# Kernel tuning notes

Measured on AMD Instinct MI355X. Metric: run time of the kernel, lower is better.

## Reference

```python
import jax, jax.numpy as jnp
import numpy as np

B, S, D, H = 4, 2048, 1024, 16
HD = D // H          # head_dim = 64; per-head scale = sqrt(HD) as in source
FF = 4096
EPS = 1e-5


def _layernorm(x, g, b):
    m = jnp.mean(x, axis=-1, keepdims=True)
    v = jnp.mean(jnp.square(x - m), axis=-1, keepdims=True)
    return (x - m) * jax.lax.rsqrt(v + EPS) * g + b


def setup_inputs() -> dict:
    key = jax.random.key(0)
    ks = jax.random.split(key, 10)
    std = 0.02
    return {
        "x": jax.random.normal(ks[0], (B, S, D), jnp.float32),
        "wq": jax.random.normal(ks[1], (H, D, HD), jnp.float32) * std,
        "bq": jnp.zeros((H, HD), jnp.float32),
        "wk": jax.random.normal(ks[2], (H, D, HD), jnp.float32) * std,
        "bk": jnp.zeros((H, HD), jnp.float32),
        "wv": jax.random.normal(ks[3], (H, D, HD), jnp.float32) * std,
        "bv": jnp.zeros((H, HD), jnp.float32),
        "wo": jax.random.normal(ks[4], (D, D), jnp.float32) * std,
        "bo": jnp.zeros((D,), jnp.float32),
        "w1": jax.random.normal(ks[5], (D, FF), jnp.float32) * std,
        "b1": jnp.zeros((FF,), jnp.float32),
        "w2": jax.random.normal(ks[6], (FF, D), jnp.float32) * std,
        "b2": jnp.zeros((D,), jnp.float32),
        "g1": jnp.ones((D,), jnp.float32),
        "beta1": jnp.zeros((D,), jnp.float32),
        "g2": jnp.ones((D,), jnp.float32),
        "beta2": jnp.zeros((D,), jnp.float32),
    }


def reference(x, wq, bq, wk, bk, wv, bv, wo, bo, w1, b1, w2, b2, g1, beta1, g2, beta2):
    # Per-head Q/K/V projections (stacked over heads) -> [B,H,S,HD]
    q = jnp.einsum('bsd,hdf->bhsf', x, wq) + bq[None, :, None, :]
    k = jnp.einsum('bsd,hdf->bhsf', x, wk) + bk[None, :, None, :]
    v = jnp.einsum('bsd,hdf->bhsf', x, wv) + bv[None, :, None, :]

    scale = jnp.sqrt(jnp.asarray(HD, jnp.float32))
    att = jnp.einsum('bhqf,bhkf->bhqk', q, k) / scale  # [B,H,S,S]
    causal = jnp.tril(jnp.ones((S, S), dtype=bool))
    att = jnp.where(causal[None, None], att, -jnp.inf)
    p = jax.nn.softmax(att, axis=-1)
    o = jnp.einsum('bhqk,bhkf->bhqf', p, v)            # [B,H,S,HD]
    o = o.transpose(0, 2, 1, 3).reshape(B, S, D)       # concat heads
    attn_out = o @ wo + bo

    h = _layernorm(x + attn_out, g1, beta1)            # post-LN, dropout=0 (eval)
    ff = jax.nn.gelu(h @ w1 + b1, approximate=False) @ w2 + b2
    return _layernorm(h + ff, g2, beta2)
```

## Files before the change

### kernel.cpp

```cpp
#include <hip/hip_runtime.h>
#include <hip/hip_bf16.h>
#include <math.h>

typedef __bf16 bf16x8 __attribute__((ext_vector_type(8)));
typedef float floatx4 __attribute__((ext_vector_type(4)));
typedef unsigned short ushort8 __attribute__((ext_vector_type(8)));
typedef unsigned short ushort4v __attribute__((ext_vector_type(4)));

__device__ __forceinline__ unsigned short f2bs(float f){
  union { float f; unsigned u; } v; v.f = f;
  unsigned r = v.u + 0x7fffu + ((v.u >> 16) & 1u);
  return (unsigned short)(r >> 16);
}
__device__ __forceinline__ float bs2f(unsigned short s){
  union { unsigned u; float f; } v; v.u = ((unsigned)s) << 16; return v.f;
}
__device__ __forceinline__ unsigned pk2(float a, float b){
  union { __hip_bfloat162 h; unsigned u; } cv;
  cv.h = __float22bfloat162_rn(make_float2(a, b));
  return cv.u;
}
__device__ __forceinline__ void gl_lds16(const void* g, void* l){
  __builtin_amdgcn_global_load_lds(
      (const __attribute__((address_space(1))) void*)g,
      (__attribute__((address_space(3))) void*)l,
      16, 0, 0);
}

__global__ __launch_bounds__(256) void cvt_x(const float* __restrict__ x,
                                             unsigned short* __restrict__ o){
  const int i = (blockIdx.x*256 + threadIdx.x)*4;
  const float4 v = *(const float4*)(x + i);
  ushort4v u = { f2bs(v.x), f2bs(v.y), f2bs(v.z), f2bs(v.w) };
  *(ushort4v*)(o + i) = u;
}

__global__ __launch_bounds__(256) void transpose_pack(const float* __restrict__ src,
                                                      unsigned short* __restrict__ dst,
                                                      int R, int C){
  __shared__ float tile[32][65];
  const int r0 = blockIdx.y*32, c0 = blockIdx.x*64;
  const int t = threadIdx.x;
  {
    const int r = t >> 3, cc = (t & 7)*8;
    const float* p = src + (size_t)(r0+r)*C + c0 + cc;
    const float4 v0 = *(const float4*)p;
    const float4 v1 = *(const float4*)(p+4);
    tile[r][cc+0]=v0.x; tile[r][cc+1]=v0.y; tile[r][cc+2]=v0.z; tile[r][cc+3]=v0.w;
    tile[r][cc+4]=v1.x; tile[r][cc+5]=v1.y; tile[r][cc+6]=v1.z; tile[r][cc+7]=v1.w;
  }
  __syncthreads();
  const int f = t >> 2, rr = (t & 3)*8;
  ushort8 u;
  #pragma unroll
  for (int j=0;j<8;j++) u[j] = f2bs(tile[rr+j][f]);
  *(ushort8*)(dst + (size_t)(c0+f)*R + r0 + rr) = u;
}

__global__ __launch_bounds__(256) void pack_qkv(const float* __restrict__ wq,
                                                const float* __restrict__ wk,
                                                const float* __restrict__ wv,
                                                const float* __restrict__ bq,
                                                const float* __restrict__ bk,
                                                const float* __restrict__ bv,
                                                unsigned short* __restrict__ Wt,
                                                float* __restrict__ Bc){
  __shared__ float tile[32][65];
  const int dt = blockIdx.x, h = blockIdx.y, sel = blockIdx.z;
  const float* src = (sel==0 ? wq : (sel==1 ? wk : wv)) + (size_t)h*65536;
  const int t = threadIdx.x, d0 = dt*32;
  {
    const int r = t >> 3, cc = (t & 7)*8;
    const float* p = src + (size_t)(d0+r)*64 + cc;
    const float4 v0 = *(const float4*)p;
    const float4 v1 = *(const float4*)(p+4);
    tile[r][cc+0]=v0.x; tile[r][cc+1]=v0.y; tile[r][cc+2]=v0.z; tile[r][cc+3]=v0.w;
    tile[r][cc+4]=v1.x; tile[r][cc+5]=v1.y; tile[r][cc+6]=v1.z; tile[r][cc+7]=v1.w;
  }
  __syncthreads();
  const int f = t >> 2, rr = (t & 3)*8;
  ushort8 u;
  #pragma unroll
  for (int j=0;j<8;j++) u[j] = f2bs(tile[rr+j][f]);
  const size_t n = (size_t)sel*1024 + h*64 + f;
  *(ushort8*)(Wt + n*1024 + d0 + rr) = u;
  if (dt==0 && t<64){
    const float* bs = (sel==0 ? bq : (sel==1 ? bk : bv)) + h*64;
    Bc[sel*1024 + h*64 + t] = bs[t];
  }
}

template<int MODE>
__global__ __launch_bounds__(256, 4)
void gemm_tn(const unsigned short* __restrict__ A,
             const unsigned short* __restrict__ Bt,
             const float* __restrict__ bias,
             void* __restrict__ out0,
             void* __restrict__ out1,
             void* __restrict__ out2,
             int K, int OW, int klen){
  __shared__ __align__(16) unsigned short As[128*32];
  __shared__ __align__(16) unsigned short Bs[128*32];
  const int tid = threadIdx.x;
  const int wave = tid >> 6, lane = tid & 63;
  const int quad = lane >> 4, l15 = lane & 15;
  const int m0 = blockIdx.x << 7, n0 = blockIdx.y << 7;
  const int kz = blockIdx.z;
  const int kbase = kz * klen;
  const int wr = (wave >> 1) << 6, wc = (wave & 1) << 6;

  floatx4 acc[4][4];
  #pragma unroll
  for (int i=0;i<4;i++)
    #pragma unroll
    for (int j=0;j<4;j++) acc[i][j] = (floatx4)0.0f;

  const unsigned short* gA[2];
  const unsigned short* gB[2];
  int lofs[2];
  #pragma unroll
  for (int r2=0;r2<2;r2++){
    const int slot = r2*256 + tid;
    const int rp = slot >> 3, rem = slot & 7;
    const int row = rp*2 + (rem >> 2);
    const int kc = (rem & 3) ^ (rp & 3);
    gA[r2] = A  + (size_t)(m0 + row)*K + kbase + kc*8;
    gB[r2] = Bt + (size_t)(n0 + row)*K + kbase + kc*8;
    lofs[r2] = slot*8;
  }
  int aofs[4], bofs[4];
  #pragma unroll
  for (int t=0;t<4;t++){
    const int ra = wr + t*16 + l15;
    aofs[t] = (ra>>1)*64 + (ra&1)*32 + ((quad ^ ((ra>>1)&3))<<3);
    const int rb = wc + t*16 + l15;
    bofs[t] = (rb>>1)*64 + (rb&1)*32 + ((quad ^ ((rb>>1)&3))<<3);
  }

  for (int k0 = 0; k0 < klen; k0 += 32){
    gl_lds16(gA[0] + k0, As + lofs[0]);
    gl_lds16(gA[1] + k0, As + lofs[1]);
    gl_lds16(gB[0] + k0, Bs + lofs[0]);
    gl_lds16(gB[1] + k0, Bs + lofs[1]);
    __syncthreads();
    bf16x8 af[4];
    #pragma unroll
    for (int t=0;t<4;t++) af[t] = *(const bf16x8*)(&As[aofs[t]]);
    #pragma unroll
    for (int j=0;j<4;j++){
      const bf16x8 bv = *(const bf16x8*)(&Bs[bofs[j]]);
      #pragma unroll
      for (int i=0;i<4;i++)
        acc[i][j] = __builtin_amdgcn_mfma_f32_16x16x32_bf16(af[i], bv, acc[i][j], 0,0,0);
    }
    __syncthreads();
  }

  #pragma unroll
  for (int i=0;i<4;i++){
    const int row0 = m0 + wr + i*16 + quad*4;
    float4 b4 = make_float4(0.f,0.f,0.f,0.f);
    if (MODE != 4 || kz == 0) b4 = *(const float4*)(bias + row0);
    #pragma unroll
    for (int j=0;j<4;j++){
      const int tok = n0 + wc + j*16 + l15;
      float v0 = acc[i][j][0] + b4.x;
      float v1 = acc[i][j][1] + b4.y;
      float v2 = acc[i][j][2] + b4.z;
      float v3 = acc[i][j][3] + b4.w;
      if (MODE == 1){
        float4 o4; o4.x=v0; o4.y=v1; o4.z=v2; o4.w=v3;
        *(float4*)((float*)out0 + (size_t)tok*OW + row0) = o4;
      } else if (MODE == 2){
        float vv[4] = {v0,v1,v2,v3};
        #pragma unroll
        for (int r=0;r<4;r++){
          const float v = vv[r];
          const float u = 0.7978845608f*v*(1.0f + 0.044715f*v*v);
          const float e = __builtin_amdgcn_exp2f(u * 2.885390082f);
          vv[r] = 0.5f*v*(1.0f + (1.0f - 2.0f/(1.0f + e)));
        }
        uint2 pkd = make_uint2(pk2(vv[0], vv[1]), pk2(vv[2], vv[3]));
        *(uint2*)((unsigned short*)out0 + (size_t)tok*4096 + row0) = pkd;
      } else if (MODE == 4){
        uint2 pkd = make_uint2(pk2(v0, v1), pk2(v2, v3));
        unsigned short* o = (unsigned short*)(kz ? out1 : out0);
        *(uint2*)(o + (size_t)tok*1024 + row0) = pkd;
      } else {
        if (row0 < 1024){
          const float s = 0.18033688011112042f;
          uint2 pkd = make_uint2(pk2(v0*s, v1*s), pk2(v2*s, v3*s));
          *(uint2*)((unsigned short*)out0 + (size_t)tok*1024 + row0) = pkd;
        } else if (row0 < 2048){
          uint2 pkd = make_uint2(pk2(v0, v1), pk2(v2, v3));
          *(uint2*)((unsigned short*)out1 + (size_t)tok*1024 + (row0-1024)) = pkd;
        } else {
          uint2 pkd = make_uint2(pk2(v0, v1), pk2(v2, v3));
          *(uint2*)((unsigned short*)out2 + (size_t)tok*1024 + (row0-2048)) = pkd;
        }
      }
    }
  }
}

__global__ __launch_bounds__(256) void vtrans(const unsigned short* __restrict__ Vtok,
                                              unsigned short* __restrict__ Vt){
  __shared__ unsigned short tile[64][65];
  const int st = blockIdx.x, bh = blockIdx.y;
  const int b = bh >> 4, h = bh & 15;
  const int t = threadIdx.x;
  {
    const int r = t >> 2, cc = (t & 3) * 16;
    const unsigned short* src = Vtok + (size_t)((b<<11) + (st<<6) + r)*1024 + (h<<6) + cc;
    ushort8 u0 = *(const ushort8*)src;
    ushort8 u1 = *(const ushort8*)(src + 8);
    #pragma unroll
    for (int j=0;j<8;j++){ tile[r][cc+j] = u0[j]; tile[r][cc+8+j] = u1[j]; }
  }
  __syncthreads();
  const int f = t >> 2, ss = (t & 3) * 16;
  ushort8 w0, w1;
  #pragma unroll
  for (int j=0;j<8;j++){ w0[j] = tile[ss+j][f]; w1[j] = tile[ss+8+j][f]; }
  unsigned short* dst = Vt + (size_t)bh*64*2048 + (size_t)f*2048 + (st<<6) + ss;
  *(ushort8*)dst = w0;
  *(ushort8*)(dst + 8) = w1;
}

__global__ __launch_bounds__(256, 4) void attn(const unsigned short* __restrict__ Q,
                                               const unsigned short* __restrict__ Kg,
                                               const unsigned short* __restrict__ Vt,
                                               unsigned short* __restrict__ O){
  __shared__ __align__(16) unsigned short Ks[64*64];
  __shared__ __align__(16) unsigned short Vs[64*64];
  __shared__ __align__(16) unsigned short PT[4][16*68];

  const int lin = blockIdx.x;
  const int bh = lin & 63;
  const int qt_lo = lin >> 6;
  const int qt_hi = 31 - qt_lo;
  const int b = bh >> 4, h = bh & 15;
  const int tid = threadIdx.x, wave = tid >> 6, lane = tid & 63;
  const int quad = lane >> 4, l15 = lane & 15;

  const size_t qbase = (size_t)((b<<11) + (wave<<4) + l15)*1024 + (h<<6);
  bf16x8 qf_hi[2], qf_lo[2];
  qf_hi[0] = *(const bf16x8*)(Q + qbase + (size_t)(qt_hi<<6)*1024 + quad*8);
  qf_hi[1] = *(const bf16x8*)(Q + qbase + (size_t)(qt_hi<<6)*1024 + 32 + quad*8);
  qf_lo[0] = *(const bf16x8*)(Q + qbase + (size_t)(qt_lo<<6)*1024 + quad*8);
  qf_lo[1] = *(const bf16x8*)(Q + qbase + (size_t)(qt_lo<<6)*1024 + 32 + quad*8);

  floatx4 oa_hi[4], oa_lo[4];
  #pragma unroll
  for (int i=0;i<4;i++){ oa_hi[i] = (floatx4)0.0f; oa_lo[i] = (floatx4)0.0f; }
  float mi_hi = -3e38f, li_hi = 0.0f;
  float mi_lo = -3e38f, li_lo = 0.0f;

  const unsigned short* Kbh = Kg + ((size_t)(b<<11))*1024 + (h<<6);
  const unsigned short* Vbh = Vt + (size_t)bh*64*2048;
  unsigned short* Pw = &PT[wave][0];

  const int slot0 = wave*128 + lane;
  const int krow0 = slot0 >> 3, kc0 = (slot0 & 7) ^ (krow0 & 7);
  const int slot1 = slot0 + 64;
  const int krow1 = slot1 >> 3, kc1 = (slot1 & 7) ^ (krow1 & 7);

  auto tile_step = [&](const bf16x8* qf, floatx4* oa, float& mi, float& li, bool diag){
    floatx4 sa[4];
    #pragma unroll
    for (int tj=0;tj<4;tj++){
      sa[tj] = (floatx4)0.0f;
      #pragma unroll
      for (int ks=0;ks<2;ks++){
        const int n = tj*16 + l15;
        const int c = (ks*4 + quad) ^ (n & 7);
        const bf16x8 kf = *(const bf16x8*)(Ks + n*64 + c*8);
        sa[tj] = __builtin_amdgcn_mfma_f32_16x16x32_bf16(kf, qf[ks], sa[tj], 0,0,0);
      }
    }
    if (diag){
      const int qrow = (wave<<4) + l15;
      #pragma unroll
      for (int tj=0;tj<4;tj++)
        #pragma unroll
        for (int r=0;r<4;r++)
          if (tj*16 + quad*4 + r > qrow) sa[tj][r] = -1e30f;
    }
    float mx = fmaxf(fmaxf(fmaxf(sa[0][0],sa[0][1]),fmaxf(sa[0][2],sa[0][3])),
                     fmaxf(fmaxf(sa[1][0],sa[1][1]),fmaxf(sa[1][2],sa[1][3])));
    mx = fmaxf(mx, fmaxf(fmaxf(fmaxf(sa[2][0],sa[2][1]),fmaxf(sa[2][2],sa[2][3])),
                         fmaxf(fmaxf(sa[3][0],sa[3][1]),fmaxf(sa[3][2],sa[3][3]))));
    mx = fmaxf(mx, __shfl_xor(mx, 16, 64));
    mx = fmaxf(mx, __shfl_xor(mx, 32, 64));
    const float mn = fmaxf(mi, mx);
    const float al = __builtin_amdgcn_exp2f(mi - mn);
    float rs = 0.0f;
    #pragma unroll
    for (int tj=0;tj<4;tj++)
      #pragma unroll
      for (int r=0;r<4;r++){
        const float p = __builtin_amdgcn_exp2f(sa[tj][r] - mn);
        sa[tj][r] = p;
        rs += p;
      }
    rs += __shfl_xor(rs, 16, 64);
    rs += __shfl_xor(rs, 32, 64);
    li = li*al + rs;
    mi = mn;
    #pragma unroll
    for (int tn=0;tn<4;tn++) oa[tn] *= al;

    #pragma unroll
    for (int tj=0;tj<4;tj++){
      uint2 pkd = make_uint2(pk2(sa[tj][0], sa[tj][1]), pk2(sa[tj][2], sa[tj][3]));
      *(uint2*)(Pw + l15*68 + tj*16 + quad*4) = pkd;
    }
    #pragma unroll
    for (int ks2=0;ks2<2;ks2++){
      const bf16x8 pf = *(const bf16x8*)(Pw + l15*68 + ks2*32 + quad*8);
      #pragma unroll
      for (int tn=0;tn<4;tn++){
        const int n2 = tn*16 + l15;
        const int c = (ks2*4 + quad) ^ (n2 & 7);
        const bf16x8 vf = *(const bf16x8*)(Vs + n2*64 + c*8);
        oa[tn] = __builtin_amdgcn_mfma_f32_16x16x32_bf16(vf, pf, oa[tn], 0,0,0);
      }
    }
  };

  for (int kt = 0; kt <= qt_hi; ++kt){
    gl_lds16(Kbh + (size_t)((kt<<6) + krow0)*1024 + kc0*8, Ks + wave*1024);
    gl_lds16(Kbh + (size_t)((kt<<6) + krow1)*1024 + kc1*8, Ks + wave*1024 + 512);
    gl_lds16(Vbh + (size_t)krow0*2048 + (kt<<6) + kc0*8, Vs + wave*1024);
    gl_lds16(Vbh + (size_t)krow1*2048 + (kt<<6) + kc1*8, Vs + wave*1024 + 512);
    __syncthreads();

    tile_step(qf_hi, oa_hi, mi_hi, li_hi, kt == qt_hi);
    if (kt <= qt_lo)
      tile_step(qf_lo, oa_lo, mi_lo, li_lo, kt == qt_lo);

    __syncthreads();
  }

  {
    const float inv = 1.0f / li_hi;
    unsigned short* Orow = O + (size_t)((b<<11) + (qt_hi<<6) + (wave<<4) + l15)*1024 + (h<<6);
    #pragma unroll
    for (int tn=0;tn<4;tn++){
      uint2 pkd = make_uint2(pk2(oa_hi[tn][0]*inv, oa_hi[tn][1]*inv),
                             pk2(oa_hi[tn][2]*inv, oa_hi[tn][3]*inv));
      *(uint2*)(Orow + tn*16 + quad*4) = pkd;
    }
  }
  {
    const float inv = 1.0f / li_lo;
    unsigned short* Orow = O + (size_t)((b<<11) + (qt_lo<<6) + (wave<<4) + l15)*1024 + (h<<6);
    #pragma unroll
    for (int tn=0;tn<4;tn++){
      uint2 pkd = make_uint2(pk2(oa_lo[tn][0]*inv, oa_lo[tn][1]*inv),
                             pk2(oa_lo[tn][2]*inv, oa_lo[tn][3]*inv));
      *(uint2*)(Orow + tn*16 + quad*4) = pkd;
    }
  }
}

__global__ __launch_bounds__(256) void ln_res(const float* __restrict__ a,
                                              const float* __restrict__ bsrc,
                                              const float* __restrict__ g,
                                              const float* __restrict__ be,
                                              float* __restrict__ of,
                                              unsigned short* __restrict__ ob){
  __shared__ float red1[4], red2[4];
  const int row = blockIdx.x, t = threadIdx.x;
  const int wave = t >> 6, lane = t & 63;
  const float4 va = *(const float4*)(a + (size_t)row*1024 + t*4);
  const float4 vb = *(const float4*)(bsrc + (size_t)row*1024 + t*4);
  float xs[4] = {va.x+vb.x, va.y+vb.y, va.z+vb.z, va.w+vb.w};
  float s = xs[0]+xs[1]+xs[2]+xs[3];
  #pragma unroll
  for (int d=1; d<64; d<<=1) s += __shfl_xor(s, d, 64);
  if (lane==0) red1[wave] = s;
  __syncthreads();
  const float mean = (red1[0]+red1[1]+red1[2]+red1[3]) * (1.0f/1024.0f);
  float vsum = 0.0f;
  #pragma unroll
  for (int i=0;i<4;i++){ const float d = xs[i]-mean; vsum += d*d; }
  #pragma unroll
  for (int d=1; d<64; d<<=1) vsum += __shfl_xor(vsum, d, 64);
  if (lane==0) red2[wave] = vsum;
  __syncthreads();
  const float var = (red2[0]+red2[1]+red2[2]+red2[3]) * (1.0f/1024.0f);
  const float rs = rsqrtf(var + 1e-5f);
  const float4 gg = *(const float4*)(g + t*4);
  const float4 bb = *(const float4*)(be + t*4);
  float y[4];
  y[0] = (xs[0]-mean)*rs*gg.x + bb.x;
  y[1] = (xs[1]-mean)*rs*gg.y + bb.y;
  y[2] = (xs[2]-mean)*rs*gg.z + bb.z;
  y[3] = (xs[3]-mean)*rs*gg.w + bb.w;
  if (of){
    float4 o4; o4.x=y[0]; o4.y=y[1]; o4.z=y[2]; o4.w=y[3];
    *(float4*)(of + (size_t)row*1024 + t*4) = o4;
  }
  if (ob){
    ushort4v u = { f2bs(y[0]), f2bs(y[1]), f2bs(y[2]), f2bs(y[3]) };
    *(ushort4v*)(ob + (size_t)row*1024 + t*4) = u;
  }
}

__global__ __launch_bounds__(256) void ln_res2(const float* __restrict__ a,
                                               const unsigned short* __restrict__ p0,
                                               const unsigned short* __restrict__ p1,
                                               const float* __restrict__ g,
                                               const float* __restrict__ be,
                                               float* __restrict__ of){
  __shared__ float red1[4], red2[4];
  const int row = blockIdx.x, t = threadIdx.x;
  const int wave = t >> 6, lane = t & 63;
  const float4 va = *(const float4*)(a + (size_t)row*1024 + t*4);
  const ushort4v u0 = *(const ushort4v*)(p0 + (size_t)row*1024 + t*4);
  const ushort4v u1 = *(const ushort4v*)(p1 + (size_t)row*1024 + t*4);
  float xs[4] = { va.x + bs2f(u0[0]) + bs2f(u1[0]),
                  va.y + bs2f(u0[1]) + bs2f(u1[1]),
                  va.z + bs2f(u0[2]) + bs2f(u1[2]),
                  va.w + bs2f(u0[3]) + bs2f(u1[3]) };
  float s = xs[0]+xs[1]+xs[2]+xs[3];
  #pragma unroll
  for (int d=1; d<64; d<<=1) s += __shfl_xor(s, d, 64);
  if (lane==0) red1[wave] = s;
  __syncthreads();
  const float mean = (red1[0]+red1[1]+red1[2]+red1[3]) * (1.0f/1024.0f);
  float vsum = 0.0f;
  #pragma unroll
  for (int i=0;i<4;i++){ const float d = xs[i]-mean; vsum += d*d; }
  #pragma unroll
  for (int d=1; d<64; d<<=1) vsum += __shfl_xor(vsum, d, 64);
  if (lane==0) red2[wave] = vsum;
  __syncthreads();
  const float var = (red2[0]+red2[1]+red2[2]+red2[3]) * (1.0f/1024.0f);
  const float rs = rsqrtf(var + 1e-5f);
  const float4 gg = *(const float4*)(g + t*4);
  const float4 bb = *(const float4*)(be + t*4);
  float4 o4;
  o4.x = (xs[0]-mean)*rs*gg.x + bb.x;
  o4.y = (xs[1]-mean)*rs*gg.y + bb.y;
  o4.z = (xs[2]-mean)*rs*gg.z + bb.z;
  o4.w = (xs[3]-mean)*rs*gg.w + bb.w;
  *(float4*)(of + (size_t)row*1024 + t*4) = o4;
}

extern "C" void kernel_launch(void* const* d_in, const int* in_sizes, int n_in,
                              void* d_out, int out_size, void* d_ws, size_t ws_size,
                              hipStream_t stream){
  (void)in_sizes; (void)n_in; (void)out_size; (void)ws_size;
  const float* x  = (const float*)d_in[0];
  const float* wq = (const float*)d_in[1];
  const float* bq = (const float*)d_in[2];
  const float* wk = (const float*)d_in[3];
  const float* bk = (const float*)d_in[4];
  const float* wv = (const float*)d_in[5];
  const float* bv = (const float*)d_in[6];
  const float* wo = (const float*)d_in[7];
  const float* bo = (const float*)d_in[8];
  const float* w1 = (const float*)d_in[9];
  const float* b1 = (const float*)d_in[10];
  const float* w2 = (const float*)d_in[11];
  const float* b2 = (const float*)d_in[12];
  const float* g1 = (const float*)d_in[13];
  const float* be1= (const float*)d_in[14];
  const float* g2 = (const float*)d_in[15];
  const float* be2= (const float*)d_in[16];
  float* out = (float*)d_out;

  char* ws = (char*)d_ws;
  size_t off = 0;
  auto take = [&](size_t bytes)->char*{
    char* p = ws + off; off += (bytes + 255) & ~(size_t)255; return p;
  };
  unsigned short* Xb  = (unsigned short*)take(8192UL*1024*2);
  unsigned short* Qb  = (unsigned short*)take(8192UL*1024*2);
  unsigned short* Kb  = (unsigned short*)take(8192UL*1024*2);
  unsigned short* Vtb = (unsigned short*)take(8192UL*1024*2);
  unsigned short* Ob  = (unsigned short*)take(8192UL*1024*2);
  unsigned short* Midb= Qb;
  unsigned short* Vtok= (unsigned short*)take(8192UL*1024*2);
  unsigned short* Wqkv= (unsigned short*)take(3072UL*1024*2);
  float*          Bqkv= (float*)take(3072UL*4);
  unsigned short* Wot = (unsigned short*)take(1024UL*1024*2);
  unsigned short* W1t = (unsigned short*)take(4096UL*1024*2);
  unsigned short* W2t = (unsigned short*)take(1024UL*4096*2);
  float*          C1  = (float*)take(8192UL*1024*4);
  unsigned short* F0  = (unsigned short*)C1;
  unsigned short* F1  = F0 + 8192UL*1024;
  float*          Hf  = (float*)take(8192UL*1024*4);
  unsigned short* Hb  = (unsigned short*)take(8192UL*1024*2);

  cvt_x<<<8192, 256, 0, stream>>>(x, Xb);
  pack_qkv<<<dim3(32,16,3), 256, 0, stream>>>(wq, wk, wv, bq, bk, bv, Wqkv, Bqkv);
  transpose_pack<<<dim3(16,32),  256, 0, stream>>>(wo, Wot, 1024, 1024);
  transpose_pack<<<dim3(64,32),  256, 0, stream>>>(w1, W1t, 1024, 4096);
  transpose_pack<<<dim3(16,128), 256, 0, stream>>>(w2, W2t, 4096, 1024);

  gemm_tn<3><<<dim3(24,64,1), 256, 0, stream>>>(Wqkv, Xb, Bqkv, Qb, Kb, Vtok, 1024, 0, 1024);
  vtrans<<<dim3(32,64), 256, 0, stream>>>(Vtok, Vtb);

  attn<<<1024, 256, 0, stream>>>(Qb, Kb, Vtb, Ob);

  gemm_tn<1><<<dim3(8,64,1), 256, 0, stream>>>(Wot, Ob, bo, C1, nullptr, nullptr, 1024, 1024, 1024);
  ln_res<<<8192, 256, 0, stream>>>(x, C1, g1, be1, Hf, Hb);

  gemm_tn<2><<<dim3(32,64,1), 256, 0, stream>>>(W1t, Hb, b1, Midb, nullptr, nullptr, 1024, 4096, 1024);
  gemm_tn<4><<<dim3(8,64,2), 256, 0, stream>>>(W2t, Midb, b2, F0, F1, nullptr, 4096, 1024, 2048);
  ln_res2<<<8192, 256, 0, stream>>>(Hf, F0, F1, g2, be2, out);
}
```

Before: 602.0 us.

## Interleave hi/lo query tiles in attention and remap GEMM block order

```diff
diff --git a/kernel.cpp b/kernel.cpp
--- a/kernel.cpp
+++ b/kernel.cpp
@@ -104,7 +104,9 @@
   const int tid = threadIdx.x;
   const int wave = tid >> 6, lane = tid & 63;
   const int quad = lane >> 4, l15 = lane & 15;
-  const int m0 = blockIdx.x << 7, n0 = blockIdx.y << 7;
+  const int lin = blockIdx.x;
+  const int n0 = (lin & 63) << 7;
+  const int m0 = (lin >> 6) << 7;
   const int kz = blockIdx.z;
   const int kbase = kz * klen;
   const int wr = (wave >> 1) << 6, wc = (wave & 1) << 6;
@@ -227,13 +229,13 @@
   *(ushort8*)(dst + 8) = w1;
 }
 
-__global__ __launch_bounds__(256, 4) void attn(const unsigned short* __restrict__ Q,
+__global__ __launch_bounds__(256, 3) void attn(const unsigned short* __restrict__ Q,
                                                const unsigned short* __restrict__ Kg,
                                                const unsigned short* __restrict__ Vt,
                                                unsigned short* __restrict__ O){
   __shared__ __align__(16) unsigned short Ks[64*64];
   __shared__ __align__(16) unsigned short Vs[64*64];
-  __shared__ __align__(16) unsigned short PT[4][16*68];
+  __shared__ __align__(16) unsigned short PT[4][2][16*68];
 
   const int lin = blockIdx.x;
   const int bh = lin & 63;
@@ -258,26 +260,16 @@
 
   const unsigned short* Kbh = Kg + ((size_t)(b<<11))*1024 + (h<<6);
   const unsigned short* Vbh = Vt + (size_t)bh*64*2048;
-  unsigned short* Pw = &PT[wave][0];
+  unsigned short* Pw0 = &PT[wave][0][0];
+  unsigned short* Pw1 = &PT[wave][1][0];
 
   const int slot0 = wave*128 + lane;
   const int krow0 = slot0 >> 3, kc0 = (slot0 & 7) ^ (krow0 & 7);
   const int slot1 = slot0 + 64;
   const int krow1 = slot1 >> 3, kc1 = (slot1 & 7) ^ (krow1 & 7);
 
-  auto tile_step = [&](const bf16x8* qf, floatx4* oa, float& mi, float& li, bool diag){
-    floatx4 sa[4];
-    #pragma unroll
-    for (int tj=0;tj<4;tj++){
-      sa[tj] = (floatx4)0.0f;
-      #pragma unroll
-      for (int ks=0;ks<2;ks++){
-        const int n = tj*16 + l15;
-        const int c = (ks*4 + quad) ^ (n & 7);
-        const bf16x8 kf = *(const bf16x8*)(Ks + n*64 + c*8);
-        sa[tj] = __builtin_amdgcn_mfma_f32_16x16x32_bf16(kf, qf[ks], sa[tj], 0,0,0);
-      }
-    }
+  auto softmax_P = [&](floatx4* sa, float& mi, float& li, floatx4* oa,
+                       unsigned short* Pbuf, bool diag){
     if (diag){
       const int qrow = (wave<<4) + l15;
       #pragma unroll
@@ -309,22 +301,10 @@
     mi = mn;
     #pragma unroll
     for (int tn=0;tn<4;tn++) oa[tn] *= al;
-
     #pragma unroll
     for (int tj=0;tj<4;tj++){
       uint2 pkd = make_uint2(pk2(sa[tj][0], sa[tj][1]), pk2(sa[tj][2], sa[tj][3]));
-      *(uint2*)(Pw + l15*68 + tj*16 + quad*4) = pkd;
-    }
-    #pragma unroll
-    for (int ks2=0;ks2<2;ks2++){
-      const bf16x8 pf = *(const bf16x8*)(Pw + l15*68 + ks2*32 + quad*8);
-      #pragma unroll
-      for (int tn=0;tn<4;tn++){
-        const int n2 = tn*16 + l15;
-        const int c = (ks2*4 + quad) ^ (n2 & 7);
-        const bf16x8 vf = *(const bf16x8*)(Vs + n2*64 + c*8);
-        oa[tn] = __builtin_amdgcn_mfma_f32_16x16x32_bf16(vf, pf, oa[tn], 0,0,0);
-      }
+      *(uint2*)(Pbuf + l15*68 + tj*16 + quad*4) = pkd;
     }
   };
 
@@ -335,10 +315,61 @@
     gl_lds16(Vbh + (size_t)krow1*2048 + (kt<<6) + kc1*8, Vs + wave*1024 + 512);
     __syncthreads();
 
-    tile_step(qf_hi, oa_hi, mi_hi, li_hi, kt == qt_hi);
-    if (kt <= qt_lo)
-      tile_step(qf_lo, oa_lo, mi_lo, li_lo, kt == qt_lo);
-
+    if (kt <= qt_lo){
+      floatx4 sh[4], sl[4];
+      #pragma unroll
+      for (int tj=0;tj<4;tj++){
+        sh[tj] = (floatx4)0.0f; sl[tj] = (floatx4)0.0f;
+        #pragma unroll
+        for (int ks=0;ks<2;ks++){
+          const int n = tj*16 + l15;
+          const int c = (ks*4 + quad) ^ (n & 7);
+          const bf16x8 kf = *(const bf16x8*)(Ks + n*64 + c*8);
+          sh[tj] = __builtin_amdgcn_mfma_f32_16x16x32_bf16(kf, qf_hi[ks], sh[tj], 0,0,0);
+          sl[tj] = __builtin_amdgcn_mfma_f32_16x16x32_bf16(kf, qf_lo[ks], sl[tj], 0,0,0);
+        }
+      }
+      softmax_P(sh, mi_hi, li_hi, oa_hi, Pw0, false);
+      softmax_P(sl, mi_lo, li_lo, oa_lo, Pw1, kt == qt_lo);
+      #pragma unroll
+      for (int ks2=0;ks2<2;ks2++){
+        const bf16x8 pfh = *(const bf16x8*)(Pw0 + l15*68 + ks2*32 + quad*8);
+        const bf16x8 pfl = *(const bf16x8*)(Pw1 + l15*68 + ks2*32 + quad*8);
+        #pragma unroll
+        for (int tn=0;tn<4;tn++){
+          const int n2 = tn*16 + l15;
+          const int c = (ks2*4 + quad) ^ (n2 & 7);
+          const bf16x8 vf = *(const bf16x8*)(Vs + n2*64 + c*8);
+          oa_hi[tn] = __builtin_amdgcn_mfma_f32_16x16x32_bf16(vf, pfh, oa_hi[tn], 0,0,0);
+          oa_lo[tn] = __builtin_amdgcn_mfma_f32_16x16x32_bf16(vf, pfl, oa_lo[tn], 0,0,0);
+        }
+      }
+    } else {
+      floatx4 sh[4];
+      #pragma unroll
+      for (int tj=0;tj<4;tj++){
+        sh[tj] = (floatx4)0.0f;
+        #pragma unroll
+        for (int ks=0;ks<2;ks++){
+          const int n = tj*16 + l15;
+          const int c = (ks*4 + quad) ^ (n & 7);
+          const bf16x8 kf = *(const bf16x8*)(Ks + n*64 + c*8);
+          sh[tj] = __builtin_amdgcn_mfma_f32_16x16x32_bf16(kf, qf_hi[ks], sh[tj], 0,0,0);
+        }
+      }
+      softmax_P(sh, mi_hi, li_hi, oa_hi, Pw0, kt == qt_hi);
+      #pragma unroll
+      for (int ks2=0;ks2<2;ks2++){
+        const bf16x8 pfh = *(const bf16x8*)(Pw0 + l15*68 + ks2*32 + quad*8);
+        #pragma unroll
+        for (int tn=0;tn<4;tn++){
+          const int n2 = tn*16 + l15;
+          const int c = (ks2*4 + quad) ^ (n2 & 7);
+          const bf16x8 vf = *(const bf16x8*)(Vs + n2*64 + c*8);
+          oa_hi[tn] = __builtin_amdgcn_mfma_f32_16x16x32_bf16(vf, pfh, oa_hi[tn], 0,0,0);
+        }
+      }
+    }
     __syncthreads();
   }
 
@@ -501,15 +532,15 @@
   transpose_pack<<<dim3(64,32),  256, 0, stream>>>(w1, W1t, 1024, 4096);
   transpose_pack<<<dim3(16,128), 256, 0, stream>>>(w2, W2t, 4096, 1024);
 
-  gemm_tn<3><<<dim3(24,64,1), 256, 0, stream>>>(Wqkv, Xb, Bqkv, Qb, Kb, Vtok, 1024, 0, 1024);
+  gemm_tn<3><<<24*64, 256, 0, stream>>>(Wqkv, Xb, Bqkv, Qb, Kb, Vtok, 1024, 0, 1024);
   vtrans<<<dim3(32,64), 256, 0, stream>>>(Vtok, Vtb);
 
   attn<<<1024, 256, 0, stream>>>(Qb, Kb, Vtb, Ob);
 
-  gemm_tn<1><<<dim3(8,64,1), 256, 0, stream>>>(Wot, Ob, bo, C1, nullptr, nullptr, 1024, 1024, 1024);
+  gemm_tn<1><<<8*64, 256, 0, stream>>>(Wot, Ob, bo, C1, nullptr, nullptr, 1024, 1024, 1024);
   ln_res<<<8192, 256, 0, stream>>>(x, C1, g1, be1, Hf, Hb);
 
-  gemm_tn<2><<<dim3(32,64,1), 256, 0, stream>>>(W1t, Hb, b1, Midb, nullptr, nullptr, 1024, 4096, 1024);
-  gemm_tn<4><<<dim3(8,64,2), 256, 0, stream>>>(W2t, Midb, b2, F0, F1, nullptr, 4096, 1024, 2048);
+  gemm_tn<2><<<32*64, 256, 0, stream>>>(W1t, Hb, b1, Midb, nullptr, nullptr, 1024, 4096, 1024);
+  gemm_tn<4><<<dim3(8*64,1,2), 256, 0, stream>>>(W2t, Midb, b2, F0, F1, nullptr, 4096, 1024, 2048);
   ln_res2<<<8192, 256, 0, stream>>>(Hf, F0, F1, g2, be2, out);
 }
```

New measurement: 568.4 us. -5.6%, faster.
